# Performance work log

Hardware: AMD Instinct MI355X
Metric: run time of the kernel (lower is better)

## Reference

```python
import jax, jax.numpy as jnp
import numpy as np

B, T, C = 2, 2048, 1024
N_HEAD = 16
HEAD_DIM = C // N_HEAD


def setup_inputs() -> dict:
    key = jax.random.key(0)
    k1, k2, k3 = jax.random.split(key, 3)
    x = jax.random.normal(k1, (B, T, C), dtype=jnp.float32)
    w_attn = jax.random.normal(k2, (C, 3 * C), dtype=jnp.float32) * 0.02
    b_attn = jnp.zeros((3 * C,), dtype=jnp.float32)
    w_proj = jax.random.normal(k3, (C, C), dtype=jnp.float32) * 0.02
    b_proj = jnp.zeros((C,), dtype=jnp.float32)
    return {"x": x, "w_attn": w_attn, "b_attn": b_attn, "w_proj": w_proj, "b_proj": b_proj}


def reference(x, w_attn, b_attn, w_proj, b_proj):
    Bz, Tz, Cz = x.shape
    qkv = x @ w_attn + b_attn                       # [B, T, 3C]
    q, k, v = jnp.split(qkv, 3, axis=-1)
    # [B, H, T, D]
    q = q.reshape(Bz, Tz, N_HEAD, HEAD_DIM).transpose(0, 2, 1, 3)
    k = k.reshape(Bz, Tz, N_HEAD, HEAD_DIM).transpose(0, 2, 1, 3)
    v = v.reshape(Bz, Tz, N_HEAD, HEAD_DIM).transpose(0, 2, 1, 3)
    scale = 1.0 / np.sqrt(HEAD_DIM).astype(np.float32)
    att = jnp.einsum('bhqd,bhkd->bhqk', q, k) * scale  # [B, H, T, T]
    causal = jnp.tril(jnp.ones((Tz, Tz), dtype=bool))
    att = jnp.where(causal[None, None], att, -jnp.inf)
    att = jax.nn.softmax(att, axis=-1)
    y = jnp.einsum('bhqk,bhkd->bhqd', att, v)          # [B, H, T, D]
    y = y.transpose(0, 2, 1, 3).reshape(Bz, Tz, Cz)
    return y @ w_proj + b_proj
```

## Files before the change

### kernel.cpp

```cpp
#include <hip/hip_runtime.h>
#include <stdint.h>

#define T_SEQ 2048
#define NH 16
#define HD 64
#define M_DIM 4096
#define K_DIM 1024

typedef __attribute__((ext_vector_type(8))) short bf16x8;
typedef __attribute__((ext_vector_type(4))) float f32x4;
typedef __attribute__((ext_vector_type(4))) unsigned short u16x4;

__device__ __forceinline__ unsigned short f2bf(float f) {
  union { float f; uint32_t u; } x; x.f = f;
  uint32_t u = x.u;
  return (unsigned short)((u + 0x7fffu + ((u >> 16) & 1u)) >> 16);
}

__device__ __forceinline__ uint32_t cvtpk_bf16(float a, float b) {
  uint32_t r;
  asm("v_cvt_pk_bf16_f32 %0, %1, %2" : "=v"(r) : "v"(a), "v"(b));
  return r;
}

#define GLOAD16(g, l) __builtin_amdgcn_global_load_lds( \
    (const __attribute__((address_space(1))) unsigned int*)(g), \
    (__attribute__((address_space(3))) unsigned int*)(l), 16, 0, 0)

__global__ __launch_bounds__(256) void convert_x_kernel(const float* __restrict__ src,
                                                        unsigned short* __restrict__ dst) {
  int idx = (blockIdx.x * 256 + threadIdx.x) * 4;
  f32x4 v = *(const f32x4*)(src + idx);
  u16x4 o;
  #pragma unroll
  for (int i = 0; i < 4; ++i) o[i] = f2bf(v[i]);
  *(u16x4*)(dst + idx) = o;
}

__global__ __launch_bounds__(256) void transpose_w_kernel(const float* __restrict__ src,
                                                          unsigned short* __restrict__ dst,
                                                          int R, int Cn) {
  __shared__ float tile[64][65];
  const int r0 = blockIdx.y * 64, c0 = blockIdx.x * 64;
  const int t = threadIdx.x;
  const int rr = t >> 4;
  const int c4 = (t & 15) * 4;
  #pragma unroll
  for (int p = 0; p < 4; ++p) {
    f32x4 v = *(const f32x4*)(src + (size_t)(r0 + p * 16 + rr) * Cn + c0 + c4);
    #pragma unroll
    for (int i = 0; i < 4; ++i) tile[p * 16 + rr][c4 + i] = v[i];
  }
  __syncthreads();
  #pragma unroll
  for (int p = 0; p < 4; ++p) {
    const int cl = p * 16 + rr;
    u16x4 o;
    #pragma unroll
    for (int i = 0; i < 4; ++i) o[i] = f2bf(tile[c4 + i][cl]);
    *(u16x4*)(dst + (size_t)(c0 + cl) * R + r0 + c4) = o;
  }
}

template <int MODE>
__global__ __launch_bounds__(256) void gemm_bt_kernel(
    const unsigned short* __restrict__ A,
    const unsigned short* __restrict__ Bt,
    const float* __restrict__ bias,
    unsigned short* __restrict__ qout,
    unsigned short* __restrict__ kout,
    unsigned short* __restrict__ vTout,
    float* __restrict__ fout) {
  __shared__ __align__(16) unsigned short As[128 * 32];
  __shared__ __align__(16) unsigned short Bs[128 * 32];
  const int t = threadIdx.x;
  const int w = t >> 6, l = t & 63;
  const int wr = w >> 1, wc = w & 1;
  const int lr = l & 15, lg = l >> 4;
  const int br = blockIdx.y, bc = blockIdx.x;

  f32x4 acc[4][4];
  const f32x4 zf = {0.f, 0.f, 0.f, 0.f};
  #pragma unroll
  for (int i = 0; i < 4; ++i)
    #pragma unroll
    for (int j = 0; j < 4; ++j) acc[i][j] = zf;

  const int ce = (t & 3) * 8;
  const unsigned short* Abase = A + (size_t)(br * 128) * K_DIM;
  const unsigned short* Bbase = Bt + (size_t)(bc * 128) * K_DIM;

  for (int k0 = 0; k0 < K_DIM; k0 += 32) {
    #pragma unroll
    for (int it = 0; it < 2; ++it) {
      const int u = it * 256 + t;
      const int row = u >> 2;
      GLOAD16(Abase + (size_t)row * K_DIM + k0 + ce, As + u * 8);
      GLOAD16(Bbase + (size_t)row * K_DIM + k0 + ce, Bs + u * 8);
    }
    __syncthreads();
    bf16x8 af[4], bfv[4];
    #pragma unroll
    for (int f = 0; f < 4; ++f) {
      af[f]  = *(const bf16x8*)(As + (wr * 64 + f * 16 + lr) * 32 + lg * 8);
      bfv[f] = *(const bf16x8*)(Bs + (wc * 64 + f * 16 + lr) * 32 + lg * 8);
    }
    #pragma unroll
    for (int fr = 0; fr < 4; ++fr)
      #pragma unroll
      for (int fc = 0; fc < 4; ++fc)
        acc[fr][fc] = __builtin_amdgcn_mfma_f32_16x16x32_bf16(af[fr], bfv[fc], acc[fr][fc], 0, 0, 0);
    __syncthreads();
  }

  #pragma unroll
  for (int fr = 0; fr < 4; ++fr) {
    #pragma unroll
    for (int fc = 0; fc < 4; ++fc) {
      const int m0 = br * 128 + wr * 64 + fr * 16 + lg * 4;
      const int n  = bc * 128 + wc * 64 + fc * 16 + lr;
      if (MODE == 0) {
        const int which = n >> 10, rem = n & 1023;
        const int h = rem >> 6, d = rem & 63;
        const int b = m0 >> 11, tt0 = m0 & 2047;
        const int bh = b * NH + h;
        if (which == 2) {
          u16x4 pack;
          #pragma unroll
          for (int r = 0; r < 4; ++r) pack[r] = f2bf(acc[fr][fc][r] + bias[n]);
          *(u16x4*)(vTout + ((size_t)bh * HD + d) * T_SEQ + tt0) = pack;
        } else {
          unsigned short* o = (which == 0) ? qout : kout;
          const float sc = (which == 0) ? 0.18033688011112042f : 1.0f;
          #pragma unroll
          for (int r = 0; r < 4; ++r)
            o[((size_t)bh * T_SEQ + tt0 + r) * HD + d] = f2bf((acc[fr][fc][r] + bias[n]) * sc);
        }
      } else {
        #pragma unroll
        for (int r = 0; r < 4; ++r)
          fout[(size_t)(m0 + r) * 1024 + n] = acc[fr][fc][r] + bias[n];
      }
    }
  }
}

__global__ __launch_bounds__(256) void flash_attn_kernel(
    const unsigned short* __restrict__ qg,
    const unsigned short* __restrict__ kg,
    const unsigned short* __restrict__ vTg,
    unsigned short* __restrict__ yg) {
  __shared__ __align__(16) unsigned short Ks[2][64 * 64];
  __shared__ __align__(16) unsigned short Vs[2][64 * 64];
  __shared__ __align__(16) unsigned short P[4][16][64];

  const int t = threadIdx.x;
  const int w = t >> 6, l = t & 63;
  const int lr = l & 15, lg = l >> 4;
  const int lb = (blockIdx.x & 7) * 64 + (blockIdx.x >> 3);
  const int pid = lb & 15;
  const int bh = lb >> 4;
  const int swz = lr & 7;

  const int srow0 = t >> 3;
  const int sch = t & 7;

  const size_t kgb = (size_t)bh * T_SEQ * HD;
  const size_t vgb = (size_t)bh * HD * T_SEQ;
  const f32x4 zf = {0.f, 0.f, 0.f, 0.f};

  #pragma unroll 1
  for (int ph = 0; ph < 2; ++ph) {
    const int qt = ph ? (31 - pid) : pid;
    const int nt = qt + 1;
    const int qw = qt * 64 + w * 16;
    const int qrow = qw + lr;

    const size_t qoff = ((size_t)bh * T_SEQ + qw + lr) * HD + lg * 8;
    const bf16x8 qf0 = *(const bf16x8*)(qg + qoff);
    const bf16x8 qf1 = *(const bf16x8*)(qg + qoff + 32);

    f32x4 acc[4];
    #pragma unroll
    for (int i = 0; i < 4; ++i) acc[i] = zf;
    float m_run = 0.f;
    float l_part = 0.f;

    #pragma unroll
    for (int sh = 0; sh < 2; ++sh) {
      const int row = sh * 32 + srow0;
      const int sc = (sch ^ (row & 7)) * 8;
      GLOAD16(kg + kgb + (size_t)row * HD + sc, Ks[0] + row * 64 + sch * 8);
      GLOAD16(vTg + vgb + (size_t)row * T_SEQ + sc, Vs[0] + row * 64 + sch * 8);
    }
    __syncthreads();

    int cur = 0;
    #pragma unroll 1
    for (int it = 0; it < nt; ++it) {
      const int kv0 = it * 64;
      if (it + 1 < nt) {
        const int kvn = kv0 + 64;
        #pragma unroll
        for (int sh = 0; sh < 2; ++sh) {
          const int row = sh * 32 + srow0;
          const int sc = (sch ^ (row & 7)) * 8;
          GLOAD16(kg + kgb + (size_t)(kvn + row) * HD + sc, Ks[cur ^ 1] + row * 64 + sch * 8);
          GLOAD16(vTg + vgb + (size_t)row * T_SEQ + kvn + sc, Vs[cur ^ 1] + row * 64 + sch * 8);
        }
      }

      f32x4 s[4];
      __builtin_amdgcn_s_setprio(1);
      #pragma unroll
      for (int fc = 0; fc < 4; ++fc) {
        const unsigned short* kr = Ks[cur] + (fc * 16 + lr) * 64;
        const bf16x8 k0v = *(const bf16x8*)(kr + ((lg ^ swz) * 8));
        const bf16x8 k1v = *(const bf16x8*)(kr + (((lg + 4) ^ swz) * 8));
        f32x4 sv = zf;
        sv = __builtin_amdgcn_mfma_f32_16x16x32_bf16(k0v, qf0, sv, 0, 0, 0);
        sv = __builtin_amdgcn_mfma_f32_16x16x32_bf16(k1v, qf1, sv, 0, 0, 0);
        s[fc] = sv;
      }
      __builtin_amdgcn_s_setprio(0);

      if (it == nt - 1) {
        #pragma unroll
        for (int fc = 0; fc < 4; ++fc)
          #pragma unroll
          for (int r = 0; r < 4; ++r) {
            const int tkv = kv0 + fc * 16 + lg * 4 + r;
            if (tkv > qrow) s[fc][r] = -1e30f;
          }
      }

      float mt = s[0][0];
      #pragma unroll
      for (int fc = 0; fc < 4; ++fc)
        #pragma unroll
        for (int r = 0; r < 4; ++r) mt = fmaxf(mt, s[fc][r]);
      if (__any(mt > m_run + 8.f)) {
        float mrow = fmaxf(mt, __shfl_xor(mt, 16));
        mrow = fmaxf(mrow, __shfl_xor(mrow, 32));
        const float m_new = fmaxf(m_run, mrow);
        const float fac = __builtin_amdgcn_exp2f(m_run - m_new);
        l_part *= fac;
        float frs[4];
        #pragma unroll
        for (int r = 0; r < 4; ++r) frs[r] = __shfl(fac, lg * 4 + r);
        #pragma unroll
        for (int fd = 0; fd < 4; ++fd)
          #pragma unroll
          for (int r = 0; r < 4; ++r) acc[fd][r] *= frs[r];
        m_run = m_new;
      }

      #pragma unroll
      for (int fc = 0; fc < 4; ++fc) {
        float e0 = __builtin_amdgcn_exp2f(s[fc][0] - m_run);
        float e1 = __builtin_amdgcn_exp2f(s[fc][1] - m_run);
        float e2 = __builtin_amdgcn_exp2f(s[fc][2] - m_run);
        float e3 = __builtin_amdgcn_exp2f(s[fc][3] - m_run);
        l_part += (e0 + e1) + (e2 + e3);
        uint2 pk;
        pk.x = cvtpk_bf16(e0, e1);
        pk.y = cvtpk_bf16(e2, e3);
        *(uint2*)&P[w][lr][(fc * 16 + lg * 4) ^ ((lr & 3) << 4)] = pk;
      }

      const bf16x8 pa0 = *(const bf16x8*)&P[w][lr][(lg * 8) ^ ((lr & 3) << 4)];
      const bf16x8 pa1 = *(const bf16x8*)&P[w][lr][(32 + lg * 8) ^ ((lr & 3) << 4)];
      __builtin_amdgcn_s_setprio(1);
      #pragma unroll
      for (int fd = 0; fd < 4; ++fd) {
        const unsigned short* vr = Vs[cur] + (fd * 16 + lr) * 64;
        const bf16x8 v0 = *(const bf16x8*)(vr + ((lg ^ swz) * 8));
        const bf16x8 v1 = *(const bf16x8*)(vr + (((lg + 4) ^ swz) * 8));
        acc[fd] = __builtin_amdgcn_mfma_f32_16x16x32_bf16(pa0, v0, acc[fd], 0, 0, 0);
        acc[fd] = __builtin_amdgcn_mfma_f32_16x16x32_bf16(pa1, v1, acc[fd], 0, 0, 0);
      }
      __builtin_amdgcn_s_setprio(0);
      __syncthreads();
      cur ^= 1;
    }

    float lsum = l_part;
    lsum += __shfl_xor(lsum, 16);
    lsum += __shfl_xor(lsum, 32);

    const int b = bh >> 4, h = bh & 15;
    #pragma unroll
    for (int r = 0; r < 4; ++r) {
      const float lv = __shfl(lsum, lg * 4 + r);
      const float linv = 1.f / lv;
      const int tt = qw + lg * 4 + r;
      #pragma unroll
      for (int fd = 0; fd < 4; ++fd) {
        const int d = fd * 16 + lr;
        yg[(((size_t)b * T_SEQ + tt) * NH + h) * HD + d] = f2bf(acc[fd][r] * linv);
      }
    }
    __syncthreads();
  }
}

extern "C" void kernel_launch(void* const* d_in, const int* in_sizes, int n_in,
                              void* d_out, int out_size, void* d_ws, size_t ws_size,
                              hipStream_t stream) {
  (void)in_sizes; (void)n_in; (void)out_size; (void)ws_size;
  const float* x      = (const float*)d_in[0];
  const float* w_attn = (const float*)d_in[1];
  const float* b_attn = (const float*)d_in[2];
  const float* w_proj = (const float*)d_in[3];
  const float* b_proj = (const float*)d_in[4];
  float* out = (float*)d_out;

  char* ws = (char*)d_ws;
  unsigned short* xb     = (unsigned short*)(ws);
  unsigned short* wqkvT  = (unsigned short*)(ws + (8ull  << 20));
  unsigned short* wprojT = (unsigned short*)(ws + (14ull << 20));
  unsigned short* qb     = (unsigned short*)(ws + (16ull << 20));
  unsigned short* kb     = (unsigned short*)(ws + (24ull << 20));
  unsigned short* vT     = (unsigned short*)(ws + (32ull << 20));
  unsigned short* yb     = (unsigned short*)(ws + (40ull << 20));

  convert_x_kernel<<<4096, 256, 0, stream>>>(x, xb);
  transpose_w_kernel<<<dim3(48, 16), 256, 0, stream>>>(w_attn, wqkvT, 1024, 3072);
  transpose_w_kernel<<<dim3(16, 16), 256, 0, stream>>>(w_proj, wprojT, 1024, 1024);
  gemm_bt_kernel<0><<<dim3(24, 32), 256, 0, stream>>>(xb, wqkvT, b_attn, qb, kb, vT, nullptr);
  flash_attn_kernel<<<512, 256, 0, stream>>>(qb, kb, vT, yb);
  gemm_bt_kernel<1><<<dim3(8, 32), 256, 0, stream>>>(yb, wprojT, b_proj, nullptr, nullptr, nullptr, out);
}
```

Measured before the change: 202.2 us.

## Fuse prep kernels, double-buffer GEMM LDS, and enlarge QKV GEMM tile

Merges the x conversion and both weight transposes into one launch to cut launch overhead. Rewrites the GEMM with double-buffered LDS so global-to-LDS loads for the next K slice overlap MFMA work on the current one. The QKV GEMM now uses 256-row tiles with 512 threads, giving more reuse of each B tile. The trade-offs are doubled LDS use and fewer blocks (384) for the QKV GEMM, which may lower occupancy.

```diff
diff --git a/kernel.cpp b/kernel.cpp
--- a/kernel.cpp
+++ b/kernel.cpp
@@ -27,9 +27,9 @@
     (const __attribute__((address_space(1))) unsigned int*)(g), \
     (__attribute__((address_space(3))) unsigned int*)(l), 16, 0, 0)
 
-__global__ __launch_bounds__(256) void convert_x_kernel(const float* __restrict__ src,
-                                                        unsigned short* __restrict__ dst) {
-  int idx = (blockIdx.x * 256 + threadIdx.x) * 4;
+__device__ __forceinline__ void do_convert(const float* __restrict__ src,
+                                           unsigned short* __restrict__ dst, int bid) {
+  int idx = (bid * 256 + threadIdx.x) * 4;
   f32x4 v = *(const f32x4*)(src + idx);
   u16x4 o;
   #pragma unroll
@@ -37,11 +37,11 @@
   *(u16x4*)(dst + idx) = o;
 }
 
-__global__ __launch_bounds__(256) void transpose_w_kernel(const float* __restrict__ src,
-                                                          unsigned short* __restrict__ dst,
-                                                          int R, int Cn) {
-  __shared__ float tile[64][65];
-  const int r0 = blockIdx.y * 64, c0 = blockIdx.x * 64;
+__device__ __forceinline__ void do_transpose(const float* __restrict__ src,
+                                             unsigned short* __restrict__ dst,
+                                             int R, int Cn, int bx, int by,
+                                             float (*tile)[65]) {
+  const int r0 = by * 64, c0 = bx * 64;
   const int t = threadIdx.x;
   const int rr = t >> 4;
   const int c4 = (t & 15) * 4;
@@ -62,8 +62,25 @@
   }
 }
 
-template <int MODE>
-__global__ __launch_bounds__(256) void gemm_bt_kernel(
+__global__ __launch_bounds__(256) void prep_kernel(
+    const float* __restrict__ x, unsigned short* __restrict__ xb,
+    const float* __restrict__ w_attn, unsigned short* __restrict__ wqkvT,
+    const float* __restrict__ w_proj, unsigned short* __restrict__ wprojT) {
+  __shared__ float tile[64][65];
+  const int b = blockIdx.x;
+  if (b < 4096) {
+    do_convert(x, xb, b);
+  } else if (b < 4096 + 768) {
+    const int bid = b - 4096;
+    do_transpose(w_attn, wqkvT, 1024, 3072, bid % 48, bid / 48, tile);
+  } else {
+    const int bid = b - 4864;
+    do_transpose(w_proj, wprojT, 1024, 1024, bid % 16, bid / 16, tile);
+  }
+}
+
+template <int MODE, int WM>
+__global__ __launch_bounds__(WM * 128) void gemm2_kernel(
     const unsigned short* __restrict__ A,
     const unsigned short* __restrict__ Bt,
     const float* __restrict__ bias,
@@ -71,8 +88,12 @@
     unsigned short* __restrict__ kout,
     unsigned short* __restrict__ vTout,
     float* __restrict__ fout) {
-  __shared__ __align__(16) unsigned short As[128 * 32];
-  __shared__ __align__(16) unsigned short Bs[128 * 32];
+  constexpr int BM = WM * 64;
+  constexpr int NT = WM * 128;
+  constexpr int U_A = BM * 4;
+  constexpr int NU = (U_A + 512) / NT;
+  __shared__ __align__(16) unsigned short As[2][BM * 32];
+  __shared__ __align__(16) unsigned short Bs[2][128 * 32];
   const int t = threadIdx.x;
   const int w = t >> 6, l = t & 63;
   const int wr = w >> 1, wc = w & 1;
@@ -86,38 +107,58 @@
     #pragma unroll
     for (int j = 0; j < 4; ++j) acc[i][j] = zf;
 
-  const int ce = (t & 3) * 8;
-  const unsigned short* Abase = A + (size_t)(br * 128) * K_DIM;
+  const unsigned short* Abase = A + (size_t)(br * BM) * K_DIM;
   const unsigned short* Bbase = Bt + (size_t)(bc * 128) * K_DIM;
 
-  for (int k0 = 0; k0 < K_DIM; k0 += 32) {
-    #pragma unroll
-    for (int it = 0; it < 2; ++it) {
-      const int u = it * 256 + t;
-      const int row = u >> 2;
-      GLOAD16(Abase + (size_t)row * K_DIM + k0 + ce, As + u * 8);
-      GLOAD16(Bbase + (size_t)row * K_DIM + k0 + ce, Bs + u * 8);
-    }
+  #define STAGE(k0, buf) do {                                                    \
+    _Pragma("unroll")                                                            \
+    for (int i = 0; i < NU; ++i) {                                               \
+      const int u = i * NT + t;                                                  \
+      if (u < U_A) {                                                             \
+        GLOAD16(Abase + (size_t)(u >> 2) * K_DIM + (k0) + (u & 3) * 8,           \
+                &As[buf][u * 8]);                                                \
+      } else {                                                                   \
+        const int v = u - U_A;                                                   \
+        GLOAD16(Bbase + (size_t)(v >> 2) * K_DIM + (k0) + (v & 3) * 8,           \
+                &Bs[buf][v * 8]);                                                \
+      }                                                                          \
+    }                                                                            \
+  } while (0)
+
+  #define COMPUTE(buf) do {                                                      \
+    bf16x8 af[4], bfv[4];                                                        \
+    _Pragma("unroll")                                                            \
+    for (int f = 0; f < 4; ++f) {                                                \
+      af[f]  = *(const bf16x8*)(&As[buf][(wr * 64 + f * 16 + lr) * 32 + lg * 8]);\
+      bfv[f] = *(const bf16x8*)(&Bs[buf][(wc * 64 + f * 16 + lr) * 32 + lg * 8]);\
+    }                                                                            \
+    _Pragma("unroll")                                                            \
+    for (int fr = 0; fr < 4; ++fr)                                               \
+      _Pragma("unroll")                                                          \
+      for (int fc = 0; fc < 4; ++fc)                                             \
+        acc[fr][fc] = __builtin_amdgcn_mfma_f32_16x16x32_bf16(af[fr], bfv[fc],   \
+                                                              acc[fr][fc], 0, 0, 0); \
+  } while (0)
+
+  STAGE(0, 0);
+  __syncthreads();
+  #pragma unroll 1
+  for (int k0 = 0; k0 < K_DIM; k0 += 64) {
+    if (k0 + 32 < K_DIM) STAGE(k0 + 32, 1);
+    COMPUTE(0);
     __syncthreads();
-    bf16x8 af[4], bfv[4];
-    #pragma unroll
-    for (int f = 0; f < 4; ++f) {
-      af[f]  = *(const bf16x8*)(As + (wr * 64 + f * 16 + lr) * 32 + lg * 8);
-      bfv[f] = *(const bf16x8*)(Bs + (wc * 64 + f * 16 + lr) * 32 + lg * 8);
-    }
-    #pragma unroll
-    for (int fr = 0; fr < 4; ++fr)
-      #pragma unroll
-      for (int fc = 0; fc < 4; ++fc)
-        acc[fr][fc] = __builtin_amdgcn_mfma_f32_16x16x32_bf16(af[fr], bfv[fc], acc[fr][fc], 0, 0, 0);
+    if (k0 + 64 < K_DIM) STAGE(k0 + 64, 0);
+    COMPUTE(1);
     __syncthreads();
   }
+  #undef STAGE
+  #undef COMPUTE
 
   #pragma unroll
   for (int fr = 0; fr < 4; ++fr) {
     #pragma unroll
     for (int fc = 0; fc < 4; ++fc) {
-      const int m0 = br * 128 + wr * 64 + fr * 16 + lg * 4;
+      const int m0 = br * BM + wr * 64 + fr * 16 + lg * 4;
       const int n  = bc * 128 + wc * 64 + fc * 16 + lr;
       if (MODE == 0) {
         const int which = n >> 10, rem = n & 1023;
@@ -324,10 +365,8 @@
   unsigned short* vT     = (unsigned short*)(ws + (32ull << 20));
   unsigned short* yb     = (unsigned short*)(ws + (40ull << 20));
 
-  convert_x_kernel<<<4096, 256, 0, stream>>>(x, xb);
-  transpose_w_kernel<<<dim3(48, 16), 256, 0, stream>>>(w_attn, wqkvT, 1024, 3072);
-  transpose_w_kernel<<<dim3(16, 16), 256, 0, stream>>>(w_proj, wprojT, 1024, 1024);
-  gemm_bt_kernel<0><<<dim3(24, 32), 256, 0, stream>>>(xb, wqkvT, b_attn, qb, kb, vT, nullptr);
+  prep_kernel<<<5120, 256, 0, stream>>>(x, xb, w_attn, wqkvT, w_proj, wprojT);
+  gemm2_kernel<0, 4><<<dim3(24, 16), 512, 0, stream>>>(xb, wqkvT, b_attn, qb, kb, vT, nullptr);
   flash_attn_kernel<<<512, 256, 0, stream>>>(qb, kb, vT, yb);
-  gemm_bt_kernel<1><<<dim3(8, 32), 256, 0, stream>>>(yb, wprojT, b_proj, nullptr, nullptr, nullptr, out);
-}
+  gemm2_kernel<1, 2><<<dim3(8, 32), 256, 0, stream>>>(yb, wprojT, b_proj, nullptr, nullptr, nullptr, out);
+}
```

Result: faster. 189.9 us (-6.1%).
